# Kernel tuning notes

Measured on AMD Instinct MI355X. Metric: run time of the kernel, lower is better.

Reference implementation:

```python
import jax, jax.numpy as jnp
import numpy as np

EPS = 1e-5

def conv(x, w, b, pad):
    y = jax.lax.conv_general_dilated(x, w, (1, 1), [(pad, pad), (pad, pad)],
                                     dimension_numbers=('NCHW', 'OIHW', 'NCHW'))
    return y + b[None, :, None, None]

def bn(x, g, be, m, v):
    return g[None, :, None, None] * (x - m[None, :, None, None]) * jax.lax.rsqrt(v[None, :, None, None] + EPS) + be[None, :, None, None]

def haar_dwt2(x):
    # pywt db1 dwt2 on even-sized images: per 2x2 block [[a,b],[c,d]]
    # cA=(a+b+c+d)/2, cH=(a+b-c-d)/2, cV=(a-b+c-d)/2, cD=(a-b-c+d)/2
    B, C, H, W = x.shape
    xr = x.reshape(B, C, H // 2, 2, W // 2, 2)
    a = xr[:, :, :, 0, :, 0]; b = xr[:, :, :, 0, :, 1]
    c = xr[:, :, :, 1, :, 0]; d = xr[:, :, :, 1, :, 1]
    cA = (a + b + c + d) * 0.5
    cH = (a + b - c - d) * 0.5
    cV = (a - b + c - d) * 0.5
    cD = (a - b - c + d) * 0.5
    return jnp.stack([cA, cH, cV, cD], axis=2)  # [B,C,4,H/2,W/2]

def setup_inputs() -> dict:
    key = jax.random.key(0)
    ks = iter(jax.random.split(key, 64))
    def w(shape, s=0.05):
        return jax.random.normal(next(ks), shape, dtype=jnp.float32) * s
    def vecs(c):  # gamma, beta, running_mean, running_var
        return (w((c,), 0.1) + 1.0, w((c,), 0.1), w((c,), 0.1),
                jax.random.uniform(next(ks), (c,), dtype=jnp.float32) + 0.5)
    inp = {'x': jax.random.normal(next(ks), (16, 3, 512, 512), dtype=jnp.float32)}
    inp['cw1'] = w((16, 3, 1, 1)); inp['cb1'] = w((16,))
    inp['cw2'] = w((3, 16, 1, 1)); inp['cb2'] = w((3,))
    inp['lw1'] = w((64, 3, 3, 3)); inp['lb1'] = w((64,))
    inp['lg1'], inp['lbe1'], inp['lm1'], inp['lv1'] = vecs(64)
    inp['lw2'] = w((128, 64, 3, 3)); inp['lb2'] = w((128,))
    inp['lg2'], inp['lbe2'], inp['lm2'], inp['lv2'] = vecs(128)
    inp['hw1'] = w((64, 9, 3, 3)); inp['hb1'] = w((64,))
    inp['hg1'], inp['hbe1'], inp['hm1'], inp['hv1'] = vecs(64)
    inp['hw2'] = w((128, 64, 3, 3)); inp['hb2'] = w((128,))
    inp['hg2'], inp['hbe2'], inp['hm2'], inp['hv2'] = vecs(128)
    inp['fw1'] = w((128, 256, 1, 1)); inp['fb1'] = w((128,))
    inp['fg1'], inp['fbe1'], inp['fm1'], inp['fv1'] = vecs(128)
    inp['fw2'] = w((64, 128, 1, 1)); inp['fb2'] = w((64,))
    inp['fg2'], inp['fbe2'], inp['fm2'], inp['fv2'] = vecs(64)
    return inp

def reference(x, cw1, cb1, cw2, cb2,
              lw1, lb1, lg1, lbe1, lm1, lv1, lw2, lb2, lg2, lbe2, lm2, lv2,
              hw1, hb1, hg1, hbe1, hm1, hv1, hw2, hb2, hg2, hbe2, hm2, hv2,
              fw1, fb1, fg1, fbe1, fm1, fv1, fw2, fb2, fg2, fbe2, fm2, fv2):
    hsv = conv(jax.nn.relu(conv(x, cw1, cb1, 0)), cw2, cb2, 0)
    coeffs = haar_dwt2(hsv)  # [B,3,4,H/2,W/2]
    B, C, _, H, W = coeffs.shape
    low = coeffs[:, :, 0]                                   # [B,3,H,W]
    high = coeffs[:, :, 1:].reshape(B, C * 3, H, W)         # [B,9,H,W]
    lf = jax.nn.relu(bn(conv(low, lw1, lb1, 1), lg1, lbe1, lm1, lv1))
    lf = jax.nn.relu(bn(conv(lf, lw2, lb2, 1), lg2, lbe2, lm2, lv2))
    hf = jax.nn.relu(bn(conv(high, hw1, hb1, 1), hg1, hbe1, hm1, hv1))
    hf = jax.nn.relu(bn(conv(hf, hw2, hb2, 1), hg2, hbe2, hm2, hv2))
    f = jnp.concatenate([lf, hf], axis=1)                   # [B,256,H,W]
    f = jax.nn.relu(bn(conv(f, fw1, fb1, 0), fg1, fbe1, fm1, fv1))
    f = jax.nn.relu(bn(conv(f, fw2, fb2, 0), fg2, fbe2, fm2, fv2))
    return f
```

## Files before the change

kernel.cpp:

```cpp
#include <hip/hip_runtime.h>
#include <hip/hip_bf16.h>


#define EPS_BN 1e-5f

typedef unsigned int u32;
typedef unsigned short u16;
typedef __attribute__((ext_vector_type(8))) short short8;
typedef __attribute__((ext_vector_type(4))) float f32x4;

__device__ __forceinline__ u16 f2bf(float f) {
  u32 u = __float_as_uint(f);
  u32 r = (u + 0x7fffu + ((u >> 16) & 1u)) >> 16;
  return (u16)r;
}

__global__ __launch_bounds__(256) void repack_pack_kernel(
    const float* __restrict__ w, const float* __restrict__ bias,
    const float* __restrict__ g, const float* __restrict__ be,
    const float* __restrict__ m, const float* __restrict__ v,
    u16* __restrict__ wpk, float* __restrict__ brep,
    int CIN, int KHW, int COUT)
{
  int idx = blockIdx.x * 256 + threadIdx.x;
  int K = CIN * KHW * KHW;
  if (idx < K * COUT) {
    int oc = idx % COUT;
    int k  = idx / COUT;
    int ic = k % CIN;
    int kidx = k / CIN;
    int ky = kidx / KHW, kx = kidx % KHW;
    float alpha = g[oc] * rsqrtf(v[oc] + EPS_BN);
    float val = w[(((size_t)oc * CIN + ic) * KHW + ky) * KHW + kx] * alpha;
    int ks = k >> 5, c = (k >> 3) & 3, e = k & 7;
    wpk[((size_t)((ks * 4 + c) * COUT + oc)) * 8 + e] = f2bf(val);
  }
  if (idx < COUT) {
    float alpha = g[idx] * rsqrtf(v[idx] + EPS_BN);
    brep[idx] = fmaf(bias[idx], alpha, be[idx] - m[idx] * alpha);
  }
}

__global__ __launch_bounds__(256) void repack_pad_pack_kernel(
    const float* __restrict__ w, const float* __restrict__ bias,
    const float* __restrict__ g, const float* __restrict__ be,
    const float* __restrict__ m, const float* __restrict__ v,
    u16* __restrict__ wpk, float* __restrict__ brep, int CIN, int COUT)
{
  int idx = blockIdx.x * 256 + threadIdx.x;
  if (idx < 160 * COUT) {
    int oc = idx % COUT;
    int k  = idx / COUT;
    int kidx = k >> 4, ic = k & 15;
    float val = 0.f;
    if (kidx < 9 && ic < CIN) {
      int ky = kidx / 3, kx = kidx % 3;
      float alpha = g[oc] * rsqrtf(v[oc] + EPS_BN);
      val = w[(((size_t)oc * CIN + ic) * 3 + ky) * 3 + kx] * alpha;
    }
    int ks = k >> 5, c = (k >> 3) & 3, e = k & 7;
    wpk[((size_t)((ks * 4 + c) * COUT + oc)) * 8 + e] = f2bf(val);
  }
  if (idx < COUT) {
    float alpha = g[idx] * rsqrtf(v[idx] + EPS_BN);
    brep[idx] = fmaf(bias[idx], alpha, be[idx] - m[idx] * alpha);
  }
}

__global__ __launch_bounds__(256) void front_kernel(
    const float* __restrict__ x,
    const float* __restrict__ cw1, const float* __restrict__ cb1,
    const float* __restrict__ cw2, const float* __restrict__ cb2,
    u16* __restrict__ low16, u16* __restrict__ high16)
{
  const int pid = blockIdx.x * 256 + threadIdx.x;
  const int wo = pid & 255, ho = (pid >> 8) & 255, b = pid >> 16;
  float hsv[2][2][3];
  #pragma unroll
  for (int dy = 0; dy < 2; ++dy) {
    #pragma unroll
    for (int dx = 0; dx < 2; ++dx) {
      int h = 2 * ho + dy, w = 2 * wo + dx;
      size_t base = ((size_t)(b * 3) << 18) + (size_t)h * 512 + w;
      float p0 = x[base];
      float p1 = x[base + (1u << 18)];
      float p2 = x[base + (2u << 18)];
      float o0 = cb2[0], o1 = cb2[1], o2 = cb2[2];
      #pragma unroll
      for (int o = 0; o < 16; ++o) {
        float t = fmaf(cw1[o*3+2], p2, fmaf(cw1[o*3+1], p1, fmaf(cw1[o*3+0], p0, cb1[o])));
        t = fmaxf(t, 0.f);
        o0 = fmaf(cw2[o],      t, o0);
        o1 = fmaf(cw2[16 + o], t, o1);
        o2 = fmaf(cw2[32 + o], t, o2);
      }
      hsv[dy][dx][0] = o0; hsv[dy][dx][1] = o1; hsv[dy][dx][2] = o2;
    }
  }
  u16 lrec[16], hrec[16];
  #pragma unroll
  for (int i = 0; i < 16; ++i) { lrec[i] = 0; hrec[i] = 0; }
  #pragma unroll
  for (int c = 0; c < 3; ++c) {
    float a  = hsv[0][0][c], bb = hsv[0][1][c];
    float cc = hsv[1][0][c], dd = hsv[1][1][c];
    lrec[c]         = f2bf((a + bb + cc + dd) * 0.5f);
    hrec[c * 3 + 0] = f2bf((a + bb - cc - dd) * 0.5f);
    hrec[c * 3 + 1] = f2bf((a - bb + cc - dd) * 0.5f);
    hrec[c * 3 + 2] = f2bf((a - bb - cc + dd) * 0.5f);
  }
  *(uint4*)(low16  + (size_t)pid * 16)     = *(const uint4*)&lrec[0];
  *(uint4*)(low16  + (size_t)pid * 16 + 8) = *(const uint4*)&lrec[8];
  *(uint4*)(high16 + (size_t)pid * 16)     = *(const uint4*)&hrec[0];
  *(uint4*)(high16 + (size_t)pid * 16 + 8) = *(const uint4*)&hrec[8];
}

__global__ __launch_bounds__(256) void conv3x3s_mfma(
    const u16* __restrict__ in16, const u16* __restrict__ wpk,
    const float* __restrict__ brep, u16* __restrict__ out)
{
  __shared__ __align__(16) u16 smem[3 * 130 * 24];
  u16 (*Arow)[130][24] = (u16(*)[130][24])smem;

  const int tid = threadIdx.x;
  const int l = tid & 63, wid = tid >> 6;
  const int bid = blockIdx.x;
  const int swz = (bid & 7) * 1024 + (bid >> 3);
  const int xh = swz & 1, h = (swz >> 1) & 255, b = swz >> 9;
  const int w0 = xh * 128;
  const int pixW = (wid >> 1) * 64, n0 = (wid & 1) * 32;
  const int lr = l & 15, lc = l >> 4;

  for (int i = tid; i < 3 * 130 * 2; i += 256) {
    int half = i & 1, rec = i >> 1;
    int px = rec % 130, row = rec / 130;
    int gy = h + row - 1, gx = w0 + px - 1;
    uint4 vv = make_uint4(0, 0, 0, 0);
    if ((unsigned)gy < 256u && (unsigned)gx < 256u)
      vv = *(const uint4*)(in16 + ((size_t)((b * 256 + gy) * 256 + gx)) * 16 + half * 8);
    *(uint4*)&Arow[row][px][half * 8] = vv;
  }
  __syncthreads();

  f32x4 acc[4][2];
  #pragma unroll
  for (int m = 0; m < 4; ++m)
    #pragma unroll
    for (int n = 0; n < 2; ++n)
      #pragma unroll
      for (int j = 0; j < 4; ++j) acc[m][n][j] = 0.f;

  const short8* wpk8 = (const short8*)wpk;
  #pragma unroll
  for (int s = 0; s < 5; ++s) {
    int kidx = s * 2 + (lc >> 1);
    int ky = (kidx < 9) ? (kidx / 3) : 0;
    int kx = (kidx < 9) ? (kidx % 3) : 0;
    int chb = (lc & 1) * 8;
    short8 a[4], bf[2];
    #pragma unroll
    for (int m = 0; m < 4; ++m)
      a[m] = *(const short8*)&Arow[ky][pixW + m * 16 + lr + kx][chb];
    #pragma unroll
    for (int n = 0; n < 2; ++n)
      bf[n] = wpk8[(s * 4 + lc) * 64 + n0 + n * 16 + lr];
    #pragma unroll
    for (int m = 0; m < 4; ++m)
      #pragma unroll
      for (int n = 0; n < 2; ++n)
        acc[m][n] = __builtin_amdgcn_mfma_f32_16x16x32_bf16(a[m], bf[n], acc[m][n], 0, 0, 0);
  }

  __syncthreads();
  u16 (*soutp)[72] = (u16(*)[72])smem;
  #pragma unroll
  for (int n = 0; n < 2; ++n) {
    const int oc = n0 + n * 16 + lr;
    const float bs = brep[oc];
    #pragma unroll
    for (int m = 0; m < 4; ++m)
      #pragma unroll
      for (int j = 0; j < 4; ++j)
        soutp[pixW + m * 16 + lc * 4 + j][oc] = f2bf(fmaxf(acc[m][n][j] + bs, 0.f));
  }
  __syncthreads();
  const size_t rowbase = (size_t)((b * 256 + h) * 256 + w0);
  for (int i = tid; i < 128 * 8; i += 256) {
    int c = i & 7, px = i >> 3;
    *(uint4*)(out + (rowbase + px) * 64 + c * 8) = *(const uint4*)&soutp[px][c * 8];
  }
}

__global__ __launch_bounds__(256, 2) void conv3x3_mfma(
    const u16* __restrict__ in, const u16* __restrict__ wpk,
    const float* __restrict__ brep, u16* __restrict__ out,
    int out_stride, int out_choff)
{
  __shared__ __align__(16) unsigned char smem[3 * 8 * 133 * 16];
  uint4 (*Arow)[8][133] = (uint4(*)[8][133])smem;

  const int tid = threadIdx.x;
  const int l = tid & 63, wid = tid >> 6;
  const int bid = blockIdx.x;
  const int swz = (bid & 7) * 1024 + (bid >> 3);
  const int xh = swz & 1, h = (swz >> 1) & 255, b = swz >> 9;
  const int w0 = xh * 128;

  const int waveM = wid >> 1, waveN = wid & 1;
  const int pixW = waveM * 64, n0 = waveN * 64;
  const int lr = l & 15, lc = l >> 4;

  for (int i = tid; i < 3 * 130 * 8; i += 256) {
    int c = i & 7;
    int t = i >> 3;
    int px = t % 130;
    int row = t / 130;
    int gy = h + row - 1, gx = w0 + px - 1;
    uint4 vv = make_uint4(0, 0, 0, 0);
    if ((unsigned)gy < 256u && (unsigned)gx < 256u)
      vv = *(const uint4*)(in + ((size_t)((b * 256 + gy) * 256 + gx)) * 64 + c * 8);
    Arow[row][c][px] = vv;
  }
  __syncthreads();

  f32x4 acc[4][4];
  #pragma unroll
  for (int m = 0; m < 4; ++m)
    #pragma unroll
    for (int n = 0; n < 4; ++n)
      #pragma unroll
      for (int j = 0; j < 4; ++j) acc[m][n][j] = 0.f;

  const short8* wpk8 = (const short8*)wpk;
  #pragma unroll
  for (int kidx = 0; kidx < 9; ++kidx) {
    const int ky = kidx / 3, kx = kidx % 3;
    #pragma unroll
    for (int cs = 0; cs < 2; ++cs) {
      short8 a[4], bf[4];
      #pragma unroll
      for (int m = 0; m < 4; ++m)
        a[m] = *(const short8*)&Arow[ky][cs * 4 + lc][pixW + m * 16 + lr + kx];
      #pragma unroll
      for (int n = 0; n < 4; ++n)
        bf[n] = wpk8[((kidx * 2 + cs) * 4 + lc) * 128 + n0 + n * 16 + lr];
      #pragma unroll
      for (int m = 0; m < 4; ++m)
        #pragma unroll
        for (int n = 0; n < 4; ++n)
          acc[m][n] = __builtin_amdgcn_mfma_f32_16x16x32_bf16(a[m], bf[n], acc[m][n], 0, 0, 0);
    }
  }

  __syncthreads();
  u16 (*soutp)[136] = (u16(*)[136])smem;
  #pragma unroll
  for (int n = 0; n < 4; ++n) {
    const int oc = n0 + n * 16 + lr;
    const float bs = brep[oc];
    #pragma unroll
    for (int m = 0; m < 4; ++m)
      #pragma unroll
      for (int j = 0; j < 4; ++j)
        soutp[pixW + m * 16 + lc * 4 + j][oc] = f2bf(fmaxf(acc[m][n][j] + bs, 0.f));
  }
  __syncthreads();
  const size_t rowbase = (size_t)((b * 256 + h) * 256 + w0);
  for (int i = tid; i < 128 * 16; i += 256) {
    int c = i & 15, px = i >> 4;
    *(uint4*)(out + (rowbase + px) * (size_t)out_stride + out_choff + c * 8) =
        *(const uint4*)&soutp[px][c * 8];
  }
}

__global__ __launch_bounds__(256, 2) void fuse_mfma(
    const u16* __restrict__ fcat,
    const u16* __restrict__ w1p, const float* __restrict__ b1r,
    const u16* __restrict__ w2p, const float* __restrict__ b2r,
    float* __restrict__ out)
{
  __shared__ __align__(16) uint4 smem4[32 * 65];
  const int tid = threadIdx.x;
  const int l = tid & 63, wid = tid >> 6;
  const int w0 = blockIdx.x * 64, hh = blockIdx.y, b = blockIdx.z;
  const int pixW = (wid >> 1) * 32;
  const int n0 = (wid & 1) * 64;
  const int lr = l & 15, lc = l >> 4;
  const size_t rowbase = (size_t)((b * 256 + hh) * 256 + w0);

  #pragma unroll
  for (int it = 0; it < 8; ++it) {
    int i = it * 256 + tid;
    int px = i >> 5, c = i & 31;
    smem4[c * 65 + px] = *(const uint4*)(fcat + (rowbase + px) * 256 + c * 8);
  }
  __syncthreads();

  f32x4 acc[2][4];
  #pragma unroll
  for (int m = 0; m < 2; ++m)
    #pragma unroll
    for (int n = 0; n < 4; ++n)
      #pragma unroll
      for (int j = 0; j < 4; ++j) acc[m][n][j] = 0.f;

  const short8* w1p8 = (const short8*)w1p;
  #pragma unroll
  for (int ks = 0; ks < 8; ++ks) {
    short8 a[2], bf[4];
    #pragma unroll
    for (int m = 0; m < 2; ++m)
      a[m] = *(const short8*)&smem4[(ks * 4 + lc) * 65 + pixW + m * 16 + lr];
    #pragma unroll
    for (int n = 0; n < 4; ++n)
      bf[n] = w1p8[(ks * 4 + lc) * 128 + n0 + n * 16 + lr];
    #pragma unroll
    for (int m = 0; m < 2; ++m)
      #pragma unroll
      for (int n = 0; n < 4; ++n)
        acc[m][n] = __builtin_amdgcn_mfma_f32_16x16x32_bf16(a[m], bf[n], acc[m][n], 0, 0, 0);
  }
  __syncthreads();

  u16* A2u = (u16*)smem4;
  #pragma unroll
  for (int n = 0; n < 4; ++n) {
    const int oc = n0 + n * 16 + lr;
    const float bs = b1r[oc];
    #pragma unroll
    for (int m = 0; m < 2; ++m)
      #pragma unroll
      for (int j = 0; j < 4; ++j) {
        int px = pixW + m * 16 + lc * 4 + j;
        A2u[((size_t)(oc >> 3) * 65 + px) * 8 + (oc & 7)] =
            f2bf(fmaxf(acc[m][n][j] + bs, 0.f));
      }
  }
  __syncthreads();

  const int n02 = (wid & 1) * 32;
  f32x4 acc2[2][2];
  #pragma unroll
  for (int m = 0; m < 2; ++m)
    #pragma unroll
    for (int n = 0; n < 2; ++n)
      #pragma unroll
      for (int j = 0; j < 4; ++j) acc2[m][n][j] = 0.f;

  const short8* w2p8 = (const short8*)w2p;
  #pragma unroll
  for (int ks = 0; ks < 4; ++ks) {
    short8 a[2], bf[2];
    #pragma unroll
    for (int m = 0; m < 2; ++m)
      a[m] = *(const short8*)&smem4[(ks * 4 + lc) * 65 + pixW + m * 16 + lr];
    #pragma unroll
    for (int n = 0; n < 2; ++n)
      bf[n] = w2p8[(ks * 4 + lc) * 64 + n02 + n * 16 + lr];
    #pragma unroll
    for (int m = 0; m < 2; ++m)
      #pragma unroll
      for (int n = 0; n < 2; ++n)
        acc2[m][n] = __builtin_amdgcn_mfma_f32_16x16x32_bf16(a[m], bf[n], acc2[m][n], 0, 0, 0);
  }
  __syncthreads();

  float (*sout)[65] = (float(*)[65])smem4;
  #pragma unroll
  for (int n = 0; n < 2; ++n) {
    const int oc = n02 + n * 16 + lr;
    const float bs = b2r[oc];
    #pragma unroll
    for (int m = 0; m < 2; ++m)
      #pragma unroll
      for (int j = 0; j < 4; ++j)
        sout[oc][pixW + m * 16 + lc * 4 + j] = fmaxf(acc2[m][n][j] + bs, 0.f);
  }
  __syncthreads();
  for (int i = tid; i < 64 * 64; i += 256) {
    int oc = i >> 6, px = i & 63;
    out[(((size_t)b * 64 + oc) << 16) + (size_t)hh * 256 + w0 + px] = sout[oc][px];
  }
}

extern "C" void kernel_launch(void* const* d_in, const int* in_sizes, int n_in,
                              void* d_out, int out_size, void* d_ws, size_t ws_size,
                              hipStream_t stream)
{
  const float* x   = (const float*)d_in[0];
  const float* cw1 = (const float*)d_in[1];
  const float* cb1 = (const float*)d_in[2];
  const float* cw2 = (const float*)d_in[3];
  const float* cb2 = (const float*)d_in[4];
  const float* lw1 = (const float*)d_in[5];
  const float* lb1 = (const float*)d_in[6];
  const float* lg1 = (const float*)d_in[7];
  const float* lbe1= (const float*)d_in[8];
  const float* lm1 = (const float*)d_in[9];
  const float* lv1 = (const float*)d_in[10];
  const float* lw2 = (const float*)d_in[11];
  const float* lb2 = (const float*)d_in[12];
  const float* lg2 = (const float*)d_in[13];
  const float* lbe2= (const float*)d_in[14];
  const float* lm2 = (const float*)d_in[15];
  const float* lv2 = (const float*)d_in[16];
  const float* hw1 = (const float*)d_in[17];
  const float* hb1 = (const float*)d_in[18];
  const float* hg1 = (const float*)d_in[19];
  const float* hbe1= (const float*)d_in[20];
  const float* hm1 = (const float*)d_in[21];
  const float* hv1 = (const float*)d_in[22];
  const float* hw2 = (const float*)d_in[23];
  const float* hb2 = (const float*)d_in[24];
  const float* hg2 = (const float*)d_in[25];
  const float* hbe2= (const float*)d_in[26];
  const float* hm2 = (const float*)d_in[27];
  const float* hv2 = (const float*)d_in[28];
  const float* fw1 = (const float*)d_in[29];
  const float* fb1 = (const float*)d_in[30];
  const float* fg1 = (const float*)d_in[31];
  const float* fbe1= (const float*)d_in[32];
  const float* fm1 = (const float*)d_in[33];
  const float* fv1 = (const float*)d_in[34];
  const float* fw2 = (const float*)d_in[35];
  const float* fb2 = (const float*)d_in[36];
  const float* fg2 = (const float*)d_in[37];
  const float* fbe2= (const float*)d_in[38];
  const float* fm2 = (const float*)d_in[39];
  const float* fv2 = (const float*)d_in[40];

  char* ws = (char*)d_ws;
  const size_t MB = 1024 * 1024;
  u16* lf1    = (u16*)(ws);
  u16* hf1    = (u16*)(ws + 135 * MB);
  char* regA  = ws + 270 * MB;
  u16* low16  = (u16*)(regA);
  u16* high16 = (u16*)(regA + 34 * MB);
  u16* fcat   = (u16*)(regA);
  char* wtail = regA + 538 * MB;
  size_t woff = 0;
  auto alloc = [&](size_t bytes) -> void* {
    void* p = wtail + woff;
    woff = (woff + bytes + 255) & ~(size_t)255;
    return p;
  };
  u16* wl1p = (u16*)alloc(160*64*2);    float* bl1r = (float*)alloc(64*4);
  u16* wh1p = (u16*)alloc(160*64*2);    float* bh1r = (float*)alloc(64*4);
  u16* wl2p = (u16*)alloc(576*128*2);   float* bl2r = (float*)alloc(128*4);
  u16* wh2p = (u16*)alloc(576*128*2);   float* bh2r = (float*)alloc(128*4);
  u16* wf1p = (u16*)alloc(256*128*2);   float* bf1r = (float*)alloc(128*4);
  u16* wf2p = (u16*)alloc(128*64*2);    float* bf2r = (float*)alloc(64*4);

  repack_pad_pack_kernel<<<40, 256, 0, stream>>>(lw1, lb1, lg1, lbe1, lm1, lv1, wl1p, bl1r, 3, 64);
  repack_pad_pack_kernel<<<40, 256, 0, stream>>>(hw1, hb1, hg1, hbe1, hm1, hv1, wh1p, bh1r, 9, 64);
  repack_pack_kernel<<<(576*128+255)/256, 256, 0, stream>>>(lw2, lb2, lg2, lbe2, lm2, lv2, wl2p, bl2r, 64, 3, 128);
  repack_pack_kernel<<<(576*128+255)/256, 256, 0, stream>>>(hw2, hb2, hg2, hbe2, hm2, hv2, wh2p, bh2r, 64, 3, 128);
  repack_pack_kernel<<<(256*128+255)/256, 256, 0, stream>>>(fw1, fb1, fg1, fbe1, fm1, fv1, wf1p, bf1r, 256, 1, 128);
  repack_pack_kernel<<<(128*64+255)/256,  256, 0, stream>>>(fw2, fb2, fg2, fbe2, fm2, fv2, wf2p, bf2r, 128, 1, 64);

  front_kernel<<<4096, 256, 0, stream>>>(x, cw1, cb1, cw2, cb2, low16, high16);

  conv3x3s_mfma<<<8192, 256, 0, stream>>>(low16,  wl1p, bl1r, lf1);
  conv3x3s_mfma<<<8192, 256, 0, stream>>>(high16, wh1p, bh1r, hf1);

  conv3x3_mfma<<<8192, 256, 0, stream>>>(lf1, wl2p, bl2r, fcat, 256, 0);
  conv3x3_mfma<<<8192, 256, 0, stream>>>(hf1, wh2p, bh2r, fcat, 256, 128);

  dim3 fgrid(4, 256, 16);
  fuse_mfma<<<fgrid, 256, 0, stream>>>(fcat, wf1p, bf1r, wf2p, bf2r, (float*)d_out);
}
```

Measured before the change: 1.050 ms.

## Use direct global-to-LDS loads with XOR swizzle and pipelined weight prefetch

The conv3x3 and fused 1x1 kernels now stage their input tiles with global_load_lds, which writes straight into LDS instead of going through registers. Padded border pixels are read from a small zeroed buffer. The LDS layout becomes pixel-major with an XOR channel swizzle to avoid bank conflicts, and the MFMA loops triple-buffer their weight loads two steps ahead. The second-stage weights of the fused kernel are loaded early, before the barrier. The aim is to cut register staging, address math and load latency at the cost of more VGPR pressure and a larger LDS footprint (53KB), which could reduce occupancy.

```diff
diff --git a/kernel.cpp b/kernel.cpp
--- a/kernel.cpp
+++ b/kernel.cpp
@@ -13,6 +13,12 @@
   u32 u = __float_as_uint(f);
   u32 r = (u + 0x7fffu + ((u >> 16) & 1u)) >> 16;
   return (u16)r;
+}
+
+__device__ __forceinline__ void gload_lds16(const void* g, void* l) {
+  __builtin_amdgcn_global_load_lds(
+      (const __attribute__((address_space(1))) void*)g,
+      (__attribute__((address_space(3))) void*)l, 16, 0, 0);
 }
 
 __global__ __launch_bounds__(256) void repack_pack_kernel(
@@ -194,10 +200,9 @@
 __global__ __launch_bounds__(256, 2) void conv3x3_mfma(
     const u16* __restrict__ in, const u16* __restrict__ wpk,
     const float* __restrict__ brep, u16* __restrict__ out,
-    int out_stride, int out_choff)
-{
-  __shared__ __align__(16) unsigned char smem[3 * 8 * 133 * 16];
-  uint4 (*Arow)[8][133] = (uint4(*)[8][133])smem;
+    const u16* __restrict__ zpg, int out_stride, int out_choff)
+{
+  __shared__ __align__(16) unsigned char smem[53248];
 
   const int tid = threadIdx.x;
   const int l = tid & 63, wid = tid >> 6;
@@ -205,21 +210,21 @@
   const int swz = (bid & 7) * 1024 + (bid >> 3);
   const int xh = swz & 1, h = (swz >> 1) & 255, b = swz >> 9;
   const int w0 = xh * 128;
-
-  const int waveM = wid >> 1, waveN = wid & 1;
-  const int pixW = waveM * 64, n0 = waveN * 64;
+  const int pixW = (wid >> 1) * 64, n0 = (wid & 1) * 64;
   const int lr = l & 15, lc = l >> 4;
 
-  for (int i = tid; i < 3 * 130 * 8; i += 256) {
-    int c = i & 7;
-    int t = i >> 3;
-    int px = t % 130;
-    int row = t / 130;
+  #pragma unroll
+  for (int it = 0; it < 13; ++it) {
+    int i = it * 256 + tid;
+    int row = i / 1040;
+    int rem = i - row * 1040;
+    int px = rem >> 3, cslot = rem & 7;
     int gy = h + row - 1, gx = w0 + px - 1;
-    uint4 vv = make_uint4(0, 0, 0, 0);
-    if ((unsigned)gy < 256u && (unsigned)gx < 256u)
-      vv = *(const uint4*)(in + ((size_t)((b * 256 + gy) * 256 + gx)) * 64 + c * 8);
-    Arow[row][c][px] = vv;
+    bool ok = ((unsigned)gy < 256u) && ((unsigned)gx < 256u);
+    const u16* src = ok
+        ? in + ((size_t)((b * 256 + gy) * 256 + gx)) * 64 + (cslot ^ (px & 7)) * 8
+        : zpg;
+    gload_lds16(src, smem + (size_t)i * 16);
   }
   __syncthreads();
 
@@ -232,24 +237,35 @@
       for (int j = 0; j < 4; ++j) acc[m][n][j] = 0.f;
 
   const short8* wpk8 = (const short8*)wpk;
-  #pragma unroll
-  for (int kidx = 0; kidx < 9; ++kidx) {
+  auto ldw = [&](short8* buf, int s) {
+    #pragma unroll
+    for (int n = 0; n < 4; ++n)
+      buf[n] = wpk8[(size_t)(s * 4 + lc) * 128 + n0 + n * 16 + lr];
+  };
+  auto lda = [&](short8* a, int s) {
+    const int kidx = s >> 1, cs = s & 1;
     const int ky = kidx / 3, kx = kidx % 3;
     #pragma unroll
-    for (int cs = 0; cs < 2; ++cs) {
-      short8 a[4], bf[4];
-      #pragma unroll
-      for (int m = 0; m < 4; ++m)
-        a[m] = *(const short8*)&Arow[ky][cs * 4 + lc][pixW + m * 16 + lr + kx];
+    for (int m = 0; m < 4; ++m) {
+      int px = pixW + m * 16 + lr + kx;
+      int slot = ky * 1040 + px * 8 + ((cs * 4 + lc) ^ (px & 7));
+      a[m] = *(const short8*)(smem + (size_t)slot * 16);
+    }
+  };
+
+  short8 w0b[4], w1b[4], w2b[4];
+  ldw(w0b, 0); ldw(w1b, 1);
+  #pragma unroll
+  for (int s = 0; s < 18; ++s) {
+    short8 a[4];
+    lda(a, s);
+    if (s < 16) ldw((s % 3 == 0) ? w2b : (s % 3 == 1) ? w0b : w1b, s + 2);
+    const short8* wc = (s % 3 == 0) ? w0b : (s % 3 == 1) ? w1b : w2b;
+    #pragma unroll
+    for (int m = 0; m < 4; ++m)
       #pragma unroll
       for (int n = 0; n < 4; ++n)
-        bf[n] = wpk8[((kidx * 2 + cs) * 4 + lc) * 128 + n0 + n * 16 + lr];
-      #pragma unroll
-      for (int m = 0; m < 4; ++m)
-        #pragma unroll
-        for (int n = 0; n < 4; ++n)
-          acc[m][n] = __builtin_amdgcn_mfma_f32_16x16x32_bf16(a[m], bf[n], acc[m][n], 0, 0, 0);
-    }
+        acc[m][n] = __builtin_amdgcn_mfma_f32_16x16x32_bf16(a[m], wc[n], acc[m][n], 0, 0, 0);
   }
 
   __syncthreads();
@@ -279,20 +295,22 @@
     const u16* __restrict__ w2p, const float* __restrict__ b2r,
     float* __restrict__ out)
 {
-  __shared__ __align__(16) uint4 smem4[32 * 65];
+  __shared__ __align__(16) unsigned char smem[33280];
   const int tid = threadIdx.x;
   const int l = tid & 63, wid = tid >> 6;
   const int w0 = blockIdx.x * 64, hh = blockIdx.y, b = blockIdx.z;
   const int pixW = (wid >> 1) * 32;
   const int n0 = (wid & 1) * 64;
+  const int n02 = (wid & 1) * 32;
   const int lr = l & 15, lc = l >> 4;
   const size_t rowbase = (size_t)((b * 256 + hh) * 256 + w0);
 
   #pragma unroll
   for (int it = 0; it < 8; ++it) {
     int i = it * 256 + tid;
-    int px = i >> 5, c = i & 31;
-    smem4[c * 65 + px] = *(const uint4*)(fcat + (rowbase + px) * 256 + c * 8);
+    int px = i >> 5, cslot = i & 31;
+    const u16* src = fcat + (rowbase + px) * 256 + (cslot ^ (px & 7)) * 8;
+    gload_lds16(src, smem + (size_t)i * 16);
   }
   __syncthreads();
 
@@ -305,24 +323,47 @@
       for (int j = 0; j < 4; ++j) acc[m][n][j] = 0.f;
 
   const short8* w1p8 = (const short8*)w1p;
-  #pragma unroll
-  for (int ks = 0; ks < 8; ++ks) {
-    short8 a[2], bf[4];
+  auto ldw1 = [&](short8* buf, int s) {
+    #pragma unroll
+    for (int n = 0; n < 4; ++n)
+      buf[n] = w1p8[(size_t)(s * 4 + lc) * 128 + n0 + n * 16 + lr];
+  };
+  auto lda1 = [&](short8* a, int ks) {
+    #pragma unroll
+    for (int m = 0; m < 2; ++m) {
+      int px = pixW + m * 16 + lr;
+      int slot = px * 32 + ((ks * 4 + lc) ^ (px & 7));
+      a[m] = *(const short8*)(smem + (size_t)slot * 16);
+    }
+  };
+
+  short8 w0b[4], w1b[4], w2b[4];
+  ldw1(w0b, 0); ldw1(w1b, 1);
+  #pragma unroll
+  for (int s = 0; s < 8; ++s) {
+    short8 a[2];
+    lda1(a, s);
+    if (s < 6) ldw1((s % 3 == 0) ? w2b : (s % 3 == 1) ? w0b : w1b, s + 2);
+    const short8* wc = (s % 3 == 0) ? w0b : (s % 3 == 1) ? w1b : w2b;
     #pragma unroll
     for (int m = 0; m < 2; ++m)
-      a[m] = *(const short8*)&smem4[(ks * 4 + lc) * 65 + pixW + m * 16 + lr];
-    #pragma unroll
-    for (int n = 0; n < 4; ++n)
-      bf[n] = w1p8[(ks * 4 + lc) * 128 + n0 + n * 16 + lr];
-    #pragma unroll
-    for (int m = 0; m < 2; ++m)
       #pragma unroll
       for (int n = 0; n < 4; ++n)
-        acc[m][n] = __builtin_amdgcn_mfma_f32_16x16x32_bf16(a[m], bf[n], acc[m][n], 0, 0, 0);
-  }
-  __syncthreads();
-
-  u16* A2u = (u16*)smem4;
+        acc[m][n] = __builtin_amdgcn_mfma_f32_16x16x32_bf16(a[m], wc[n], acc[m][n], 0, 0, 0);
+  }
+
+  const short8* w2p8 = (const short8*)w2p;
+  short8 wf2[4][2];
+  #pragma unroll
+  for (int ks = 0; ks < 4; ++ks)
+    #pragma unroll
+    for (int n = 0; n < 2; ++n)
+      wf2[ks][n] = w2p8[(ks * 4 + lc) * 64 + n02 + n * 16 + lr];
+
+  __syncthreads();
+
+  uint4* smem4 = (uint4*)smem;
+  u16* A2u = (u16*)smem;
   #pragma unroll
   for (int n = 0; n < 4; ++n) {
     const int oc = n0 + n * 16 + lr;
@@ -338,7 +379,6 @@
   }
   __syncthreads();
 
-  const int n02 = (wid & 1) * 32;
   f32x4 acc2[2][2];
   #pragma unroll
   for (int m = 0; m < 2; ++m)
@@ -347,25 +387,21 @@
       #pragma unroll
       for (int j = 0; j < 4; ++j) acc2[m][n][j] = 0.f;
 
-  const short8* w2p8 = (const short8*)w2p;
   #pragma unroll
   for (int ks = 0; ks < 4; ++ks) {
-    short8 a[2], bf[2];
+    short8 a[2];
     #pragma unroll
     for (int m = 0; m < 2; ++m)
       a[m] = *(const short8*)&smem4[(ks * 4 + lc) * 65 + pixW + m * 16 + lr];
     #pragma unroll
-    for (int n = 0; n < 2; ++n)
-      bf[n] = w2p8[(ks * 4 + lc) * 64 + n02 + n * 16 + lr];
-    #pragma unroll
     for (int m = 0; m < 2; ++m)
       #pragma unroll
       for (int n = 0; n < 2; ++n)
-        acc2[m][n] = __builtin_amdgcn_mfma_f32_16x16x32_bf16(a[m], bf[n], acc2[m][n], 0, 0, 0);
-  }
-  __syncthreads();
-
-  float (*sout)[65] = (float(*)[65])smem4;
+        acc2[m][n] = __builtin_amdgcn_mfma_f32_16x16x32_bf16(a[m], wf2[ks][n], acc2[m][n], 0, 0, 0);
+  }
+  __syncthreads();
+
+  float (*sout)[65] = (float(*)[65])smem;
   #pragma unroll
   for (int n = 0; n < 2; ++n) {
     const int oc = n02 + n * 16 + lr;
@@ -450,6 +486,9 @@
   u16* wh2p = (u16*)alloc(576*128*2);   float* bh2r = (float*)alloc(128*4);
   u16* wf1p = (u16*)alloc(256*128*2);   float* bf1r = (float*)alloc(128*4);
   u16* wf2p = (u16*)alloc(128*64*2);    float* bf2r = (float*)alloc(64*4);
+  u16* zpg  = (u16*)alloc(256);
+
+  hipMemsetAsync(zpg, 0, 256, stream);
 
   repack_pad_pack_kernel<<<40, 256, 0, stream>>>(lw1, lb1, lg1, lbe1, lm1, lv1, wl1p, bl1r, 3, 64);
   repack_pad_pack_kernel<<<40, 256, 0, stream>>>(hw1, hb1, hg1, hbe1, hm1, hv1, wh1p, bh1r, 9, 64);
@@ -463,8 +502,8 @@
   conv3x3s_mfma<<<8192, 256, 0, stream>>>(low16,  wl1p, bl1r, lf1);
   conv3x3s_mfma<<<8192, 256, 0, stream>>>(high16, wh1p, bh1r, hf1);
 
-  conv3x3_mfma<<<8192, 256, 0, stream>>>(lf1, wl2p, bl2r, fcat, 256, 0);
-  conv3x3_mfma<<<8192, 256, 0, stream>>>(hf1, wh2p, bh2r, fcat, 256, 128);
+  conv3x3_mfma<<<8192, 256, 0, stream>>>(lf1, wl2p, bl2r, fcat, zpg, 256, 0);
+  conv3x3_mfma<<<8192, 256, 0, stream>>>(hf1, wh2p, bh2r, fcat, zpg, 256, 128);
 
   dim3 fgrid(4, 256, 16);
   fuse_mfma<<<fgrid, 256, 0, stream>>>(fcat, wf1p, bf1r, wf2p, bf2r, (float*)d_out);
```

New measurement: 964.3 us. 1.09x faster.
